# Optimization experiments

Measured on AMD Instinct MI355X. Metric: run time of the kernel, lower is better.

The kernel has to match this reference:

```python
import jax, jax.numpy as jnp
import numpy as np

BETA = 0.25
B, N, D = 8, 4096, 256
NUM_CODES = 4096


def setup_inputs() -> dict:
    key = jax.random.key(0)
    kx, kc = jax.random.split(key)
    x = jax.random.normal(kx, (B, N, D), dtype=jnp.float32)
    # matches nn.init.uniform_(weight, -1/dim, 1/dim)
    codebook = jax.random.uniform(kc, (NUM_CODES, D), dtype=jnp.float32,
                                  minval=-1.0 / D, maxval=1.0 / D)
    return {"x": x, "codebook": codebook}


def reference(x, codebook):
    b, n, d = x.shape
    flat = x.reshape(b * n, d)                                   # [BN, D]
    # squared euclidean distances: ||z||^2 - 2 z.e^T + ||e||^2   # [BN, K]
    distances = (jnp.sum(flat * flat, axis=1, keepdims=True)
                 - 2.0 * jnp.einsum('md,kd->mk', flat, codebook)
                 + jnp.sum(codebook * codebook, axis=1)[None, :])
    indices = jnp.argmin(distances, axis=1)                      # [BN]
    z_q = codebook[indices].reshape(b, n, d)                     # [B, N, D]
    # commitment + codebook losses (detach == stop_gradient)
    sg = jax.lax.stop_gradient
    loss = jnp.mean((sg(z_q) - x) ** 2) + BETA * jnp.mean((z_q - sg(x)) ** 2)
    # straight-through estimator
    z_q_st = x + sg(z_q - x)
    return z_q_st, loss, indices.reshape(b, n)
```

## Files before the change

### kernel.cpp

```cpp
#include <hip/hip_runtime.h>

#define MTOT 32768
#define KC   4096
#define DDIM 256
#define BM   64
#define ZELEMS (MTOT * DDIM)
#define THRESH 2.0e-4f
#define WLCAP 8192
#define RGRID 2048

typedef _Float16 half8 __attribute__((ext_vector_type(8)));
typedef float f32x4 __attribute__((ext_vector_type(4)));

__device__ __forceinline__ float sqr_rn(float v) { return __fmul_rn(v, v); }

__global__ __launch_bounds__(256) void vq_prep2(const float* __restrict__ x,
                                                const float* __restrict__ cb,
                                                float* __restrict__ S,
                                                float* __restrict__ cnorm,
                                                _Float16* __restrict__ cbsw,
                                                int* __restrict__ wl_count,
                                                double* __restrict__ accum) {
  const int t = threadIdx.x;
  if (blockIdx.x == 0 && t == 0) { *accum = 0.0; *wl_count = 0; }
  const int sub = t >> 4, lane16 = t & 15;
  const int h = lane16 >> 3, j = lane16 & 7;
  const bool isrow = blockIdx.x < 2048;
  const int idx = (isrow ? blockIdx.x : blockIdx.x - 2048) * 16 + sub;
  const float* p = (isrow ? x + (size_t)idx * DDIM : cb + (size_t)idx * DDIM);

  float r = 0.f;
  const float* q = p + h * 128 + j;
#pragma unroll
  for (int i = 0; i < 16; ++i) r = __fadd_rn(r, sqr_rn(q[i * 8]));
  r = __fadd_rn(r, __shfl_xor(r, 1, 64));
  r = __fadd_rn(r, __shfl_xor(r, 2, 64));
  r = __fadd_rn(r, __shfl_xor(r, 4, 64));
  float sv = __fadd_rn(r, __shfl_xor(r, 8, 64));
  if (lane16 == 0) {
    if (isrow) S[idx] = sv; else cnorm[idx] = sv;
  }

  if (!isrow) {
    const int kt = idx >> 6, code_l = idx & 63;
    _Float16* dst0 = cbsw + (size_t)kt * 16384 + code_l * 32;
#pragma unroll
    for (int c = 0; c < 2; ++c) {
      int jj = lane16 + c * 16;
      int s = jj >> 2, hi = jj & 3;
      float4 a4 = *reinterpret_cast<const float4*>(p + jj * 8);
      float4 b4 = *reinterpret_cast<const float4*>(p + jj * 8 + 4);
      union { half8 v; _Float16 hh[8]; } u;
      u.hh[0] = (_Float16)(a4.x * 256.0f); u.hh[1] = (_Float16)(a4.y * 256.0f);
      u.hh[2] = (_Float16)(a4.z * 256.0f); u.hh[3] = (_Float16)(a4.w * 256.0f);
      u.hh[4] = (_Float16)(b4.x * 256.0f); u.hh[5] = (_Float16)(b4.y * 256.0f);
      u.hh[6] = (_Float16)(b4.z * 256.0f); u.hh[7] = (_Float16)(b4.w * 256.0f);
      *reinterpret_cast<half8*>(dst0 + s * 2048 + hi * 8) = u.v;
    }
  }
}

__global__ __launch_bounds__(256, 2) void vq_score(const float* __restrict__ x,
                                                   const _Float16* __restrict__ cbsw,
                                                   const float* __restrict__ Sarr,
                                                   const float* __restrict__ cnorm,
                                                   int* __restrict__ bestidx,
                                                   int* __restrict__ wl,
                                                   int* __restrict__ wl_count,
                                                   double* __restrict__ accum) {
  __shared__ float scrV1[4][BM];
  __shared__ float scrV2[4][BM];
  __shared__ int   scrI1[4][BM];

  const int t = threadIdx.x;
  const int m0 = blockIdx.x * BM;
  const int lane = t & 63, w = t >> 6;
  const int lo = lane & 15, hi = lane >> 4;

  half8 a[4][8];
#pragma unroll
  for (int s2 = 0; s2 < 4; ++s2) {
    const float* xr = x + (size_t)(m0 + s2 * 16 + lo) * DDIM + hi * 8;
#pragma unroll
    for (int s = 0; s < 8; ++s) {
      float4 u0 = *reinterpret_cast<const float4*>(xr + s * 32);
      float4 u1 = *reinterpret_cast<const float4*>(xr + s * 32 + 4);
      union { half8 v; _Float16 h[8]; } uu;
      uu.h[0] = (_Float16)u0.x; uu.h[1] = (_Float16)u0.y;
      uu.h[2] = (_Float16)u0.z; uu.h[3] = (_Float16)u0.w;
      uu.h[4] = (_Float16)u1.x; uu.h[5] = (_Float16)u1.y;
      uu.h[6] = (_Float16)u1.z; uu.h[7] = (_Float16)u1.w;
      a[s2][s] = uu.v;
    }
  }

  const int code_l = w * 16 + lo;
  const _Float16* bb = cbsw + w * 512 + lo * 32 + hi * 8;

  float v1[4][4], v2[4][4]; int i1[4][4];
#pragma unroll
  for (int s2 = 0; s2 < 4; ++s2)
#pragma unroll
    for (int r = 0; r < 4; ++r) { v1[s2][r] = 3.4e38f; v2[s2][r] = 3.4e38f; i1[s2][r] = 0; }

  float Ccur = cnorm[code_l];

#define BLOAD(dst, kt, s) \
  dst = *reinterpret_cast<const half8*>(bb + ((size_t)(kt) * 8 + (s)) * 2048)
#define QMFMA(buf, s0) \
  do { \
    acc[0] = __builtin_amdgcn_mfma_f32_16x16x32_f16(a[0][s0],     buf[0], acc[0], 0, 0, 0); \
    acc[1] = __builtin_amdgcn_mfma_f32_16x16x32_f16(a[1][s0],     buf[0], acc[1], 0, 0, 0); \
    acc[2] = __builtin_amdgcn_mfma_f32_16x16x32_f16(a[2][s0],     buf[0], acc[2], 0, 0, 0); \
    acc[3] = __builtin_amdgcn_mfma_f32_16x16x32_f16(a[3][s0],     buf[0], acc[3], 0, 0, 0); \
    acc[0] = __builtin_amdgcn_mfma_f32_16x16x32_f16(a[0][s0 + 1], buf[1], acc[0], 0, 0, 0); \
    acc[1] = __builtin_amdgcn_mfma_f32_16x16x32_f16(a[1][s0 + 1], buf[1], acc[1], 0, 0, 0); \
    acc[2] = __builtin_amdgcn_mfma_f32_16x16x32_f16(a[2][s0 + 1], buf[1], acc[2], 0, 0, 0); \
    acc[3] = __builtin_amdgcn_mfma_f32_16x16x32_f16(a[3][s0 + 1], buf[1], acc[3], 0, 0, 0); \
  } while (0)

  half8 bufA[2], bufB[2];
  BLOAD(bufA[0], 0, 0);
  BLOAD(bufA[1], 0, 1);

  for (int kt = 0; kt < KC / 64; ++kt) {
    const int ktn = (kt + 1) & 63;
    float Cnext = cnorm[ktn * 64 + code_l];

    f32x4 acc[4];
#pragma unroll
    for (int s2 = 0; s2 < 4; ++s2) acc[s2] = (f32x4){0.f, 0.f, 0.f, 0.f};

    BLOAD(bufB[0], kt, 2);  BLOAD(bufB[1], kt, 3);
    QMFMA(bufA, 0);
    BLOAD(bufA[0], kt, 4);  BLOAD(bufA[1], kt, 5);
    QMFMA(bufB, 2);
    BLOAD(bufB[0], kt, 6);  BLOAD(bufB[1], kt, 7);
    QMFMA(bufA, 4);
    BLOAD(bufA[0], ktn, 0); BLOAD(bufA[1], ktn, 1);
    QMFMA(bufB, 6);

    const int code = kt * 64 + code_l;
#pragma unroll
    for (int s2 = 0; s2 < 4; ++s2) {
#pragma unroll
      for (int r = 0; r < 4; ++r) {
        float sv = fmaf(acc[s2][r], -0.0078125f, Ccur);
        bool lt = sv < v1[s2][r];
        v2[s2][r] = fminf(v2[s2][r], lt ? v1[s2][r] : sv);
        if (lt) { v1[s2][r] = sv; i1[s2][r] = code; }
      }
    }
    Ccur = Cnext;
  }
#undef BLOAD
#undef QMFMA

#pragma unroll
  for (int s2 = 0; s2 < 4; ++s2) {
#pragma unroll
    for (int r = 0; r < 4; ++r) {
      float v = v1[s2][r], u = v2[s2][r]; int ii = i1[s2][r];
#pragma unroll
      for (int m = 1; m <= 8; m <<= 1) {
        float ov = __shfl_xor(v, m, 64);
        int   oi = __shfl_xor(ii, m, 64);
        float ou = __shfl_xor(u, m, 64);
        float mx = fmaxf(v, ov);
        u = fminf(fminf(u, ou), mx);
        bool take = (ov < v) || (ov == v && oi < ii);
        if (take) { v = ov; ii = oi; }
      }
      if (lo == 0) {
        int rowl = s2 * 16 + hi * 4 + r;
        scrV1[w][rowl] = v;
        scrV2[w][rowl] = u;
        scrI1[w][rowl] = ii;
      }
    }
  }
  __syncthreads();

  float part = 0.f;
  if (t < BM) {
    float bv1 = 3.4e38f, bv2 = 3.4e38f; int bi1 = 0x7fffffff;
#pragma unroll
    for (int c = 0; c < 4; ++c) {
      float v = scrV1[c][t];
      float u = scrV2[c][t];
      int  ii = scrI1[c][t];
      float mx = fmaxf(bv1, v);
      bv2 = fminf(fminf(bv2, u), mx);
      if (v < bv1 || (v == bv1 && ii < bi1)) { bv1 = v; bi1 = ii; }
    }
    int row = m0 + t;
    bestidx[row] = bi1;
    float gap = bv2 - bv1;
    if (gap <= THRESH) {
      int pos = atomicAdd(wl_count, 1);
      if (pos >= WLCAP) part = __fadd_rn(Sarr[row], bv1);
      else wl[pos] = row;
    } else {
      part = __fadd_rn(Sarr[row], bv1);
    }
  }
#pragma unroll
  for (int off = 32; off >= 1; off >>= 1) part += __shfl_down(part, off, 64);
  if (t == 0) atomicAdd(accum, (double)part);
}

__global__ __launch_bounds__(256) void vq_rescore(const float* __restrict__ x,
                                                  const float* __restrict__ cb,
                                                  const float* __restrict__ Sarr,
                                                  const float* __restrict__ cnorm,
                                                  const int* __restrict__ wl,
                                                  const int* __restrict__ wl_count,
                                                  float* __restrict__ pD,
                                                  int* __restrict__ pI) {
  const int cnt = min(*wl_count, WLCAP);
  if (cnt == 0) return;
  const int ngroups = (cnt + 3) >> 2;
  const int nitems = ngroups * 16;

  __shared__ float xs[4][260];
  __shared__ int rsh[4];
  __shared__ float scrv[4][4];
  __shared__ int   scri[4][4];

  const int t = threadIdx.x;
  const int lane = t & 63, w = t >> 6;

  for (int item = blockIdx.x; item < nitems; item += RGRID) {
    const int g = item >> 4, chunk = item & 15;
    __syncthreads();
    if (t < 4) { int e = g * 4 + t; rsh[t] = wl[(e < cnt) ? e : g * 4]; }
    __syncthreads();
    { int i = t >> 6, dq = t & 63;
      *reinterpret_cast<float4*>(&xs[i][dq * 4]) =
          *reinterpret_cast<const float4*>(x + (size_t)rsh[i] * DDIM + dq * 4); }
    __syncthreads();

    const int code = chunk * 256 + t;
    const float* cp = cb + (size_t)code * DDIM;
    const float C = cnorm[code];

    float acc[4][4];
#pragma unroll
    for (int i = 0; i < 4; ++i)
#pragma unroll
      for (int l = 0; l < 4; ++l) acc[i][l] = 0.f;

#pragma unroll 8
    for (int dq = 0; dq < 64; ++dq) {
      float4 cv = *reinterpret_cast<const float4*>(cp + dq * 4);
#pragma unroll
      for (int i = 0; i < 4; ++i) {
        float4 xv = *reinterpret_cast<float4*>(&xs[i][dq * 4]);
        acc[i][0] = __fadd_rn(acc[i][0], __fmul_rn(xv.x, cv.x));
        acc[i][1] = __fadd_rn(acc[i][1], __fmul_rn(xv.y, cv.y));
        acc[i][2] = __fadd_rn(acc[i][2], __fmul_rn(xv.z, cv.z));
        acc[i][3] = __fadd_rn(acc[i][3], __fmul_rn(xv.w, cv.w));
      }
    }

#pragma unroll
    for (int i = 0; i < 4; ++i) {
      float e = __fadd_rn(__fadd_rn(acc[i][0], acc[i][1]),
                          __fadd_rn(acc[i][2], acc[i][3]));
      float Sv = Sarr[rsh[i]];
      float D = __fadd_rn(__fsub_rn(Sv, __fmul_rn(2.0f, e)), C);
      float v = D; int ii = code;
#pragma unroll
      for (int m = 1; m <= 32; m <<= 1) {
        float ov = __shfl_xor(v, m, 64);
        int   oi = __shfl_xor(ii, m, 64);
        if (ov < v || (ov == v && oi < ii)) { v = ov; ii = oi; }
      }
      if (lane == 0) { scrv[i][w] = v; scri[i][w] = ii; }
    }
    __syncthreads();
    if (t < 4) {
      float bv = 3.4e38f; int bi = 0x7fffffff;
#pragma unroll
      for (int c = 0; c < 4; ++c) {
        float v = scrv[t][c]; int ii = scri[t][c];
        if (v < bv || (v == bv && ii < bi)) { bv = v; bi = ii; }
      }
      int rpos = g * 4 + t;
      if (rpos < cnt) { pD[rpos * 16 + chunk] = bv; pI[rpos * 16 + chunk] = bi; }
    }
  }
}

__global__ __launch_bounds__(256) void vq_combine(const int* __restrict__ wl,
                                                  const int* __restrict__ wl_count,
                                                  const float* __restrict__ pD,
                                                  const int* __restrict__ pI,
                                                  int* __restrict__ bestidx,
                                                  double* __restrict__ accum) {
  const int cnt = min(*wl_count, WLCAP);
  for (int r = blockIdx.x * 256 + threadIdx.x; r < cnt; r += gridDim.x * 256) {
    float bv = 3.4e38f; int bi = 0x7fffffff;
#pragma unroll
    for (int c = 0; c < 16; ++c) {
      float v = pD[r * 16 + c]; int ii = pI[r * 16 + c];
      if (v < bv || (v == bv && ii < bi)) { bv = v; bi = ii; }
    }
    bestidx[wl[r]] = bi;
    atomicAdd(accum, (double)bv);
  }
}

__global__ __launch_bounds__(256) void vq_emit(const float* __restrict__ x,
                                               const float* __restrict__ cb,
                                               const int* __restrict__ bestidx,
                                               float* __restrict__ out) {
  __shared__ int ish[64];
  const int t = threadIdx.x;
  const int m0 = blockIdx.x * 64;
  if (t < 64) {
    int ii = bestidx[m0 + t];
    ish[t] = ii;
    out[(size_t)ZELEMS + 1 + m0 + t] = (float)ii;
  }
  __syncthreads();
#pragma unroll
  for (int i = 0; i < 16; ++i) {
    int fi = t + i * 256;
    int row = fi >> 6, dc = fi & 63;
    int code = ish[row];
    float4 c4 = *reinterpret_cast<const float4*>(cb + (size_t)code * DDIM + dc * 4);
    float4 x4 = *reinterpret_cast<const float4*>(x + (size_t)(m0 + row) * DDIM + dc * 4);
    float4 o;
    o.x = __fadd_rn(x4.x, __fsub_rn(c4.x, x4.x));
    o.y = __fadd_rn(x4.y, __fsub_rn(c4.y, x4.y));
    o.z = __fadd_rn(x4.z, __fsub_rn(c4.z, x4.z));
    o.w = __fadd_rn(x4.w, __fsub_rn(c4.w, x4.w));
    *reinterpret_cast<float4*>(out + (size_t)(m0 + row) * DDIM + dc * 4) = o;
  }
}

__global__ void vq_final(const double* __restrict__ accum, float* __restrict__ out) {
  out[ZELEMS] = (float)(1.25 * accum[0] / (double)ZELEMS);
}

extern "C" void kernel_launch(void* const* d_in, const int* in_sizes, int n_in,
                              void* d_out, int out_size, void* d_ws, size_t ws_size,
                              hipStream_t stream) {
  const float* x  = (const float*)d_in[0];
  const float* cb = (const float*)d_in[1];
  float* out = (float*)d_out;

  char* ws = (char*)d_ws;
  float*     S        = (float*)(ws + 0);
  float*     cnorm    = (float*)(ws + 131072);
  int*       bestidx  = (int*)  (ws + 147456);
  int*       wl       = (int*)  (ws + 278528);
  int*       wl_count = (int*)  (ws + 311296);
  double*    accum    = (double*)(ws + 311312);
  float*     pD       = (float*)(ws + 315392);
  int*       pI       = (int*)  (ws + 839680);
  _Float16*  cbsw     = (_Float16*)(ws + 1363968);

  vq_prep2<<<2304, 256, 0, stream>>>(x, cb, S, cnorm, cbsw, wl_count, accum);
  vq_score<<<MTOT / BM, 256, 0, stream>>>(x, cbsw, S, cnorm, bestidx, wl, wl_count, accum);
  vq_rescore<<<RGRID, 256, 0, stream>>>(x, cb, S, cnorm, wl, wl_count, pD, pI);
  vq_combine<<<8, 256, 0, stream>>>(wl, wl_count, pD, pI, bestidx, accum);
  vq_emit<<<MTOT / 64, 256, 0, stream>>>(x, cb, bestidx, out);
  vq_final<<<1, 1, 0, stream>>>(accum, out);
}
```

Measured before the change: 198.4 us.

## Double-buffer full codebook tiles in registers with one-wave-per-SIMD occupancy

```diff
diff --git a/kernel.cpp b/kernel.cpp
--- a/kernel.cpp
+++ b/kernel.cpp
@@ -60,7 +60,7 @@
   }
 }
 
-__global__ __launch_bounds__(256, 2) void vq_score(const float* __restrict__ x,
+__global__ __launch_bounds__(256, 1) void vq_score(const float* __restrict__ x,
                                                    const _Float16* __restrict__ cbsw,
                                                    const float* __restrict__ Sarr,
                                                    const float* __restrict__ cnorm,
@@ -103,58 +103,58 @@
 #pragma unroll
     for (int r = 0; r < 4; ++r) { v1[s2][r] = 3.4e38f; v2[s2][r] = 3.4e38f; i1[s2][r] = 0; }
 
-  float Ccur = cnorm[code_l];
-
 #define BLOAD(dst, kt, s) \
   dst = *reinterpret_cast<const half8*>(bb + ((size_t)(kt) * 8 + (s)) * 2048)
-#define QMFMA(buf, s0) \
-  do { \
-    acc[0] = __builtin_amdgcn_mfma_f32_16x16x32_f16(a[0][s0],     buf[0], acc[0], 0, 0, 0); \
-    acc[1] = __builtin_amdgcn_mfma_f32_16x16x32_f16(a[1][s0],     buf[0], acc[1], 0, 0, 0); \
-    acc[2] = __builtin_amdgcn_mfma_f32_16x16x32_f16(a[2][s0],     buf[0], acc[2], 0, 0, 0); \
-    acc[3] = __builtin_amdgcn_mfma_f32_16x16x32_f16(a[3][s0],     buf[0], acc[3], 0, 0, 0); \
-    acc[0] = __builtin_amdgcn_mfma_f32_16x16x32_f16(a[0][s0 + 1], buf[1], acc[0], 0, 0, 0); \
-    acc[1] = __builtin_amdgcn_mfma_f32_16x16x32_f16(a[1][s0 + 1], buf[1], acc[1], 0, 0, 0); \
-    acc[2] = __builtin_amdgcn_mfma_f32_16x16x32_f16(a[2][s0 + 1], buf[1], acc[2], 0, 0, 0); \
-    acc[3] = __builtin_amdgcn_mfma_f32_16x16x32_f16(a[3][s0 + 1], buf[1], acc[3], 0, 0, 0); \
+
+#define TILE_BODY(buf, ktc)                                                         \
+  do {                                                                              \
+    const float C = cnorm[(ktc) * 64 + code_l];                                     \
+    f32x4 acc[4];                                                                   \
+    _Pragma("unroll")                                                               \
+    for (int s2 = 0; s2 < 4; ++s2) acc[s2] = (f32x4){0.f, 0.f, 0.f, 0.f};           \
+    _Pragma("unroll")                                                               \
+    for (int s = 0; s < 8; ++s) {                                                   \
+      acc[0] = __builtin_amdgcn_mfma_f32_16x16x32_f16(a[0][s], buf[s], acc[0], 0, 0, 0); \
+      acc[1] = __builtin_amdgcn_mfma_f32_16x16x32_f16(a[1][s], buf[s], acc[1], 0, 0, 0); \
+      acc[2] = __builtin_amdgcn_mfma_f32_16x16x32_f16(a[2][s], buf[s], acc[2], 0, 0, 0); \
+      acc[3] = __builtin_amdgcn_mfma_f32_16x16x32_f16(a[3][s], buf[s], acc[3], 0, 0, 0); \
+    }                                                                               \
+    const int code = (ktc) * 64 + code_l;                                           \
+    _Pragma("unroll")                                                               \
+    for (int s2 = 0; s2 < 4; ++s2) {                                                \
+      _Pragma("unroll")                                                             \
+      for (int r = 0; r < 4; ++r) {                                                 \
+        float sv = fmaf(acc[s2][r], -0.0078125f, C);    \
+        float mx = fmaxf(v1[s2][r], sv);                 \
+        v2[s2][r] = fminf(v2[s2][r], mx);                                           \
+        bool lt = sv < v1[s2][r];                                                   \
+        if (lt) { v1[s2][r] = sv; i1[s2][r] = code; }                               \
+      }                                                                             \
+    }                                                                               \
   } while (0)
 
-  half8 bufA[2], bufB[2];
-  BLOAD(bufA[0], 0, 0);
-  BLOAD(bufA[1], 0, 1);
-
-  for (int kt = 0; kt < KC / 64; ++kt) {
-    const int ktn = (kt + 1) & 63;
-    float Cnext = cnorm[ktn * 64 + code_l];
-
-    f32x4 acc[4];
-#pragma unroll
-    for (int s2 = 0; s2 < 4; ++s2) acc[s2] = (f32x4){0.f, 0.f, 0.f, 0.f};
-
-    BLOAD(bufB[0], kt, 2);  BLOAD(bufB[1], kt, 3);
-    QMFMA(bufA, 0);
-    BLOAD(bufA[0], kt, 4);  BLOAD(bufA[1], kt, 5);
-    QMFMA(bufB, 2);
-    BLOAD(bufB[0], kt, 6);  BLOAD(bufB[1], kt, 7);
-    QMFMA(bufA, 4);
-    BLOAD(bufA[0], ktn, 0); BLOAD(bufA[1], ktn, 1);
-    QMFMA(bufB, 6);
-
-    const int code = kt * 64 + code_l;
-#pragma unroll
-    for (int s2 = 0; s2 < 4; ++s2) {
-#pragma unroll
-      for (int r = 0; r < 4; ++r) {
-        float sv = fmaf(acc[s2][r], -0.0078125f, Ccur);
-        bool lt = sv < v1[s2][r];
-        v2[s2][r] = fminf(v2[s2][r], lt ? v1[s2][r] : sv);
-        if (lt) { v1[s2][r] = sv; i1[s2][r] = code; }
-      }
-    }
-    Ccur = Cnext;
+  half8 btA[8], btB[8];
+#pragma unroll
+  for (int s = 0; s < 8; ++s) BLOAD(btA[s], 0, s);
+#pragma unroll
+  for (int s = 0; s < 8; ++s) BLOAD(btB[s], 1, s);
+
+  for (int kt = 0; kt < KC / 64; kt += 2) {
+    TILE_BODY(btA, kt);
+    {
+      const int k2 = (kt + 2) & 63;
+#pragma unroll
+      for (int s = 0; s < 8; ++s) BLOAD(btA[s], k2, s);
+    }
+    TILE_BODY(btB, kt + 1);
+    {
+      const int k3 = (kt + 3) & 63;
+#pragma unroll
+      for (int s = 0; s < 8; ++s) BLOAD(btB[s], k3, s);
+    }
   }
 #undef BLOAD
-#undef QMFMA
+#undef TILE_BODY
 
 #pragma unroll
   for (int s2 = 0; s2 < 4; ++s2) {
```

Measured after the change: 299.1 us. 1.51x slower.
